# Performance work log

Hardware: AMD Instinct MI355X
Metric: run time of the kernel (lower is better)

## Reference

```python
import jax, jax.numpy as jnp
import numpy as np

N = 50000          # nodes
E = 1_600_000      # edges (avg degree 32)
F_IN = 128         # num_node_features
HID = 128          # hidden_dim
G = 512            # graphs in batch
NEG_SLOPE = 0.2    # PyG GATConv default


def setup_inputs() -> dict:
    key = jax.random.key(0)
    ks = jax.random.split(key, 13)
    s_in = 1.0 / np.sqrt(F_IN)
    s_h = 1.0 / np.sqrt(HID)
    return {
        "x": jax.random.normal(ks[0], (N, F_IN), jnp.float32),
        "edge_index": jax.random.randint(ks[1], (2, E), 0, N, dtype=jnp.int32),
        "batch": jnp.sort(jax.random.randint(ks[2], (N,), 0, G, dtype=jnp.int32)),
        "W1": jax.random.normal(ks[3], (F_IN, HID), jnp.float32) * s_in,
        "a_src1": jax.random.normal(ks[4], (HID,), jnp.float32) * s_h,
        "a_dst1": jax.random.normal(ks[5], (HID,), jnp.float32) * s_h,
        "b1": jnp.zeros((HID,), jnp.float32),
        "W2": jax.random.normal(ks[6], (HID, HID), jnp.float32) * s_h,
        "a_src2": jax.random.normal(ks[7], (HID,), jnp.float32) * s_h,
        "a_dst2": jax.random.normal(ks[8], (HID,), jnp.float32) * s_h,
        "b2": jnp.zeros((HID,), jnp.float32),
        "fc_w": jax.random.normal(ks[9], (2 * HID, 1), jnp.float32) * (1.0 / np.sqrt(2 * HID)),
        "fc_b": jnp.zeros((1,), jnp.float32),
    }


def _gat_conv(x, W, a_src, a_dst, b, src, dst, n):
    # PyG GATConv, heads=1: h = xW; alpha_e = softmax_dst(leaky_relu(a_s.h[src] + a_d.h[dst]))
    h = x @ W                                    # [N, C]
    asrc = h @ a_src                             # [N]
    adst = h @ a_dst                             # [N]
    logits = jax.nn.leaky_relu(asrc[src] + adst[dst], NEG_SLOPE)  # [E']
    m = jax.ops.segment_max(logits, dst, num_segments=n)
    ex = jnp.exp(logits - m[dst])
    denom = jax.ops.segment_sum(ex, dst, num_segments=n)
    alpha = ex / denom[dst]                      # segment softmax over incoming edges
    out = jax.ops.segment_sum(h[src] * alpha[:, None], dst, num_segments=n)
    return out + b


def reference(x, edge_index, batch, W1, a_src1, a_dst1, b1, W2, a_src2, a_dst2, b2, fc_w, fc_b):
    n = x.shape[0]
    loop = jnp.arange(n, dtype=edge_index.dtype)   # add_self_loops=True (PyG default)
    src = jnp.concatenate([edge_index[0], loop])
    dst = jnp.concatenate([edge_index[1], loop])

    h = jax.nn.relu(x)
    h = jax.nn.relu(_gat_conv(h, W1, a_src1, a_dst1, b1, src, dst, n))
    h = jax.nn.relu(_gat_conv(h, W2, a_src2, a_dst2, b2, src, dst, n))

    counts = jax.ops.segment_sum(jnp.ones((n,), h.dtype), batch, num_segments=G)
    maxp = jax.ops.segment_max(h, batch, num_segments=G)
    maxp = jnp.where(counts[:, None] > 0, maxp, 0.0)
    meanp = jax.ops.segment_sum(h, batch, num_segments=G) / jnp.maximum(counts, 1.0)[:, None]
    pooled = jnp.concatenate([maxp, meanp], axis=1)  # [G, 2*HID]
    return pooled @ fc_w + fc_b                      # [G, 1]
```

## Files before the change

### kernel.cpp

```cpp
#include <hip/hip_runtime.h>
#include <math.h>


#define LEAKY 0.2f
#define CAP 128
#define CSTRIDE 16

__device__ __forceinline__ unsigned short f2bf(float x) {
    unsigned int u = __float_as_uint(x);
    unsigned int r = (u + 0x7FFFu + ((u >> 16) & 1u)) >> 16;
    return (unsigned short)r;
}
__device__ __forceinline__ float bf2f(unsigned short b) {
    return __uint_as_float((unsigned int)b << 16);
}

__global__ __launch_bounds__(256) void gemmscat(const float* __restrict__ A,
                                                const float* __restrict__ B,
                                                float* __restrict__ C,
                                                unsigned short* __restrict__ Cb,
                                                const float* __restrict__ a_src,
                                                const float* __restrict__ a_dst,
                                                float* __restrict__ asv,
                                                float* __restrict__ adv,
                                                int n, int applyRelu,
                                                int gemmBlocks,
                                                const int* __restrict__ ei,
                                                int* __restrict__ cnt,
                                                unsigned short* __restrict__ col,
                                                int E) {
    __shared__ __align__(16) char smem[25600];
    float (*Ast)[68]  = (float(*)[68])smem;
    float (*Bs)[132]  = (float(*)[132])(smem + 8704);
    float (*sredS)[17] = (float(*)[17])smem;
    float (*sredD)[17] = (float(*)[17])(smem + 4352);

    if ((int)blockIdx.x >= gemmBlocks) {
        const int b = (int)blockIdx.x - gemmBlocks;
        const int g = (int)blockIdx.x & 7;
        const int lo = (int)(((long long)n * g) >> 3);
        const int hi = (int)(((long long)n * (g + 1)) >> 3);
        const int base = (b >> 3) * 4096;
        int4 dv[4], sv[4];
        int ok[4];
#pragma unroll
        for (int t = 0; t < 4; ++t) {
            int i0 = base + t * 1024 + (int)threadIdx.x * 4;
            ok[t] = (i0 < E);
            if (ok[t]) {
                dv[t] = *(const int4*)(ei + (size_t)E + i0);
                sv[t] = *(const int4*)(ei + i0);
            }
        }
#pragma unroll
        for (int t = 0; t < 4; ++t) {
            if (!ok[t]) continue;
            int dd[4] = { dv[t].x, dv[t].y, dv[t].z, dv[t].w };
            int ss[4] = { sv[t].x, sv[t].y, sv[t].z, sv[t].w };
#pragma unroll
            for (int j = 0; j < 4; ++j) {
                int d = dd[j];
                if (d >= lo && d < hi) {
                    int pos = atomicAdd(&cnt[(size_t)d * CSTRIDE], 1);
                    if (pos < CAP) col[(size_t)d * CAP + pos] = (unsigned short)ss[j];
                }
            }
        }
        return;
    }

    const int tid = threadIdx.x;
    const int row0 = blockIdx.x * 64;
    const int tx = tid & 15;
    const int ty = tid >> 4;
    float acc[4][8] = {};

    for (int k0 = 0; k0 < 128; k0 += 32) {
        {
            int kv = tid & 7, r = tid >> 3;
            int kk = kv * 4;
#pragma unroll
            for (int i = 0; i < 2; ++i) {
                int rr = r + 32 * i;
                int grow = row0 + rr;
                float4 v = make_float4(0.f, 0.f, 0.f, 0.f);
                if (grow < n) {
                    v = *(const float4*)(A + (size_t)grow * 128 + k0 + kk);
                    if (applyRelu) {
                        v.x = fmaxf(v.x, 0.f); v.y = fmaxf(v.y, 0.f);
                        v.z = fmaxf(v.z, 0.f); v.w = fmaxf(v.w, 0.f);
                    }
                }
                Ast[kk + 0][rr] = v.x;
                Ast[kk + 1][rr] = v.y;
                Ast[kk + 2][rr] = v.z;
                Ast[kk + 3][rr] = v.w;
            }
        }
        {
            int cv = tid & 31, kr = tid >> 5;
#pragma unroll
            for (int i = 0; i < 4; ++i) {
                int kk2 = kr + 8 * i;
                float4 v = *(const float4*)(B + (size_t)(k0 + kk2) * 128 + cv * 4);
                Bs[kk2][cv * 4 + 0] = v.x; Bs[kk2][cv * 4 + 1] = v.y;
                Bs[kk2][cv * 4 + 2] = v.z; Bs[kk2][cv * 4 + 3] = v.w;
            }
        }
        __syncthreads();
#pragma unroll
        for (int k = 0; k < 32; ++k) {
            float4 a4 = *(const float4*)&Ast[k][ty * 4];
            float4 q0 = *(const float4*)&Bs[k][tx * 8];
            float4 q1 = *(const float4*)&Bs[k][tx * 8 + 4];
            float a[4] = { a4.x, a4.y, a4.z, a4.w };
            float b[8] = { q0.x, q0.y, q0.z, q0.w, q1.x, q1.y, q1.z, q1.w };
#pragma unroll
            for (int i = 0; i < 4; ++i)
#pragma unroll
                for (int j = 0; j < 8; ++j) acc[i][j] += a[i] * b[j];
        }
        __syncthreads();
    }

    float asl[8], adl[8];
#pragma unroll
    for (int j = 0; j < 8; ++j) {
        asl[j] = a_src[tx * 8 + j];
        adl[j] = a_dst[tx * 8 + j];
    }
#pragma unroll
    for (int i = 0; i < 4; ++i) {
        int rr = ty * 4 + i;
        int grow = row0 + rr;
        float ps = 0.f, pd = 0.f;
#pragma unroll
        for (int j = 0; j < 8; ++j) {
            ps += acc[i][j] * asl[j];
            pd += acc[i][j] * adl[j];
        }
        sredS[rr][tx] = ps;
        sredD[rr][tx] = pd;
        if (grow < n) {
            float4* dst = (float4*)(C + (size_t)grow * 128 + tx * 8);
            dst[0] = make_float4(acc[i][0], acc[i][1], acc[i][2], acc[i][3]);
            dst[1] = make_float4(acc[i][4], acc[i][5], acc[i][6], acc[i][7]);
            uint4 pk;
            pk.x = (unsigned)f2bf(acc[i][0]) | ((unsigned)f2bf(acc[i][1]) << 16);
            pk.y = (unsigned)f2bf(acc[i][2]) | ((unsigned)f2bf(acc[i][3]) << 16);
            pk.z = (unsigned)f2bf(acc[i][4]) | ((unsigned)f2bf(acc[i][5]) << 16);
            pk.w = (unsigned)f2bf(acc[i][6]) | ((unsigned)f2bf(acc[i][7]) << 16);
            *(uint4*)(Cb + (size_t)grow * 128 + tx * 8) = pk;
        }
    }
    __syncthreads();
    if (tid < 64) {
        int grow = row0 + tid;
        if (grow < n) {
            float ps = 0.f, pd = 0.f;
#pragma unroll
            for (int j = 0; j < 16; ++j) {
                ps += sredS[tid][j];
                pd += sredD[tid][j];
            }
            asv[grow] = ps;
            adv[grow] = pd;
        }
    }
}

__global__ __launch_bounds__(256) void aggregate(const unsigned short* __restrict__ hb,
                                                 const int* __restrict__ cnt,
                                                 const unsigned short* __restrict__ col,
                                                 const float* __restrict__ asv,
                                                 const float* __restrict__ adv,
                                                 const float* __restrict__ bias,
                                                 float* __restrict__ out, int n) {
    __shared__ int   scol[4][128];
    __shared__ float swt[4][128];
    const int wv = threadIdx.x >> 6;
    const int lane = threadIdx.x & 63;
    const int w = blockIdx.x * 4 + wv;
    if (w >= n) return;
    int deg = cnt[(size_t)w * CSTRIDE];
    if (deg > CAP - 1) deg = CAP - 1;
    const int D = deg + 1;
    const size_t start = (size_t)w * CAP;
    const float ad = adv[w];

    int c0 = 0, c1 = 0;
    float l0 = -INFINITY, l1 = -INFINITY;
    if (lane < D) {
        c0 = (lane < deg) ? (int)col[start + lane] : w;
        l0 = asv[c0] + ad;
        l0 = l0 > 0.f ? l0 : LEAKY * l0;
    }
    if (64 + lane < D) {
        c1 = (64 + lane < deg) ? (int)col[start + 64 + lane] : w;
        l1 = asv[c1] + ad;
        l1 = l1 > 0.f ? l1 : LEAKY * l1;
    }
    float m = fmaxf(l0, l1);
#pragma unroll
    for (int off = 32; off; off >>= 1) m = fmaxf(m, __shfl_xor(m, off, 64));
    float e0 = (lane < D) ? __expf(l0 - m) : 0.f;
    float e1 = (64 + lane < D) ? __expf(l1 - m) : 0.f;
    float s = e0 + e1;
#pragma unroll
    for (int off = 32; off; off >>= 1) s += __shfl_xor(s, off, 64);
    float inv = 1.f / s;
    if (lane < D)      { scol[wv][lane] = c0;      swt[wv][lane] = e0; }
    if (64 + lane < D) { scol[wv][64 + lane] = c1; swt[wv][64 + lane] = e1; }

    const int hw = lane >> 5;
    const int sl = lane & 31;
    float4 aa[8];
#pragma unroll
    for (int j = 0; j < 8; ++j) aa[j] = make_float4(0.f, 0.f, 0.f, 0.f);
    for (int i = 0; i < D; i += 16) {
        int cs[8]; float ws[8];
#pragma unroll
        for (int j = 0; j < 8; ++j) {
            int idx = i + 2 * j + hw;
            int cl = idx < D ? idx : D - 1;
            cs[j] = scol[wv][cl];
            ws[j] = (idx < D) ? swt[wv][idx] : 0.f;
        }
        ushort4 rs[8];
#pragma unroll
        for (int j = 0; j < 8; ++j)
            rs[j] = *((const ushort4*)(hb + (size_t)cs[j] * 128) + sl);
#pragma unroll
        for (int j = 0; j < 8; ++j) {
            aa[j].x += ws[j] * bf2f(rs[j].x);
            aa[j].y += ws[j] * bf2f(rs[j].y);
            aa[j].z += ws[j] * bf2f(rs[j].z);
            aa[j].w += ws[j] * bf2f(rs[j].w);
        }
    }
#pragma unroll
    for (int j = 1; j < 8; ++j) {
        aa[0].x += aa[j].x; aa[0].y += aa[j].y;
        aa[0].z += aa[j].z; aa[0].w += aa[j].w;
    }
    aa[0].x += __shfl_xor(aa[0].x, 32);
    aa[0].y += __shfl_xor(aa[0].y, 32);
    aa[0].z += __shfl_xor(aa[0].z, 32);
    aa[0].w += __shfl_xor(aa[0].w, 32);
    if (hw == 0) {
        float4 b = ((const float4*)bias)[sl];
        float4 o;
        o.x = fmaxf(aa[0].x * inv + b.x, 0.f);
        o.y = fmaxf(aa[0].y * inv + b.y, 0.f);
        o.z = fmaxf(aa[0].z * inv + b.z, 0.f);
        o.w = fmaxf(aa[0].w * inv + b.w, 0.f);
        *((float4*)(out + (size_t)w * 128) + sl) = o;
    }
}

__global__ __launch_bounds__(128) void poolfc(const float* __restrict__ h2,
                                              const int* __restrict__ batch,
                                              const float* __restrict__ fcw,
                                              const float* __restrict__ fcb,
                                              float* __restrict__ out, int G, int n) {
    __shared__ int seg[2];
    int g = blockIdx.x;
    int f = threadIdx.x;
    if (f < 2) {
        int target = g + f;
        int lo = 0, hi = n;
        while (lo < hi) {
            int mid = (lo + hi) >> 1;
            if (batch[mid] < target) lo = mid + 1; else hi = mid;
        }
        seg[f] = lo;
    }
    __syncthreads();
    int s = seg[0], e = seg[1];
    float m = -INFINITY, sum = 0.f;
    for (int node = s; node < e; ++node) {
        float v = h2[(size_t)node * 128 + f];
        m = fmaxf(m, v);
        sum += v;
    }
    int cnt = e - s;
    float maxp = (cnt > 0) ? m : 0.f;
    float cden = (float)(cnt > 0 ? cnt : 1);
    float meanp = sum / cden;
    float p = maxp * fcw[f] + meanp * fcw[128 + f];
    __shared__ float red[128];
    red[f] = p;
    __syncthreads();
    for (int off = 64; off; off >>= 1) {
        if (f < off) red[f] += red[f + off];
        __syncthreads();
    }
    if (f == 0) out[g] = red[0] + fcb[0];
}

extern "C" void kernel_launch(void* const* d_in, const int* in_sizes, int n_in,
                              void* d_out, int out_size, void* d_ws, size_t ws_size,
                              hipStream_t stream) {
    const int N = in_sizes[0] / 128;
    const int E = in_sizes[1] / 2;
    const int G = out_size;

    const float* x      = (const float*)d_in[0];
    const int*   ei     = (const int*)d_in[1];
    const int*   batch  = (const int*)d_in[2];
    const float* W1     = (const float*)d_in[3];
    const float* a_src1 = (const float*)d_in[4];
    const float* a_dst1 = (const float*)d_in[5];
    const float* b1     = (const float*)d_in[6];
    const float* W2     = (const float*)d_in[7];
    const float* a_src2 = (const float*)d_in[8];
    const float* a_dst2 = (const float*)d_in[9];
    const float* b2     = (const float*)d_in[10];
    const float* fcw    = (const float*)d_in[11];
    const float* fcb    = (const float*)d_in[12];
    float* out = (float*)d_out;

    char* wp = (char*)d_ws;
    auto alloc = [&](size_t bytes) -> void* {
        void* p = (void*)wp;
        wp += (bytes + 255) & ~(size_t)255;
        return p;
    };
    int* cnt     = (int*)alloc(sizeof(int) * (size_t)N * CSTRIDE);
    unsigned short* col = (unsigned short*)alloc(sizeof(unsigned short) * (size_t)N * CAP);
    float* hp    = (float*)alloc(sizeof(float) * (size_t)N * 128);
    float* ha    = (float*)alloc(sizeof(float) * (size_t)N * 128);
    unsigned short* hb = (unsigned short*)alloc(sizeof(unsigned short) * (size_t)N * 128);
    float* asv   = (float*)alloc(sizeof(float) * N);
    float* adv   = (float*)alloc(sizeof(float) * N);

    hipMemsetAsync(cnt, 0, sizeof(int) * (size_t)N * CSTRIDE, stream);

    const int gemmGrid = (N + 63) / 64;
    const int waveGrid = (N + 3) / 4;
    const int scatGrid = ((E + 4095) / 4096) * 8;

    gemmscat<<<gemmGrid + scatGrid, 256, 0, stream>>>(
        x, W1, hp, hb, a_src1, a_dst1, asv, adv, N, 1, gemmGrid, ei, cnt, col, E);
    aggregate<<<waveGrid, 256, 0, stream>>>(hb, cnt, col, asv, adv, b1, ha, N);

    gemmscat<<<gemmGrid, 256, 0, stream>>>(
        ha, W2, hp, hb, a_src2, a_dst2, asv, adv, N, 0, gemmGrid, ei, cnt, col, E);
    aggregate<<<waveGrid, 256, 0, stream>>>(hb, cnt, col, asv, adv, b2, ha, N);

    poolfc<<<G, 128, 0, stream>>>(ha, batch, fcw, fcb, out, G, N);
}
```

Baseline: 359.3 us.

## Replace FP32 FMA GEMM with split-bf16 MFMA and drop fp32 h output

Result: faster. 352.0 us (-2.0%).

```diff
diff --git a/kernel.cpp b/kernel.cpp
--- a/kernel.cpp
+++ b/kernel.cpp
@@ -5,6 +5,9 @@
 #define LEAKY 0.2f
 #define CAP 128
 #define CSTRIDE 16
+
+typedef short bf16x8 __attribute__((ext_vector_type(8)));
+typedef float f32x4 __attribute__((ext_vector_type(4)));
 
 __device__ __forceinline__ unsigned short f2bf(float x) {
     unsigned int u = __float_as_uint(x);
@@ -15,25 +18,20 @@
     return __uint_as_float((unsigned int)b << 16);
 }
 
-__global__ __launch_bounds__(256) void gemmscat(const float* __restrict__ A,
-                                                const float* __restrict__ B,
-                                                float* __restrict__ C,
-                                                unsigned short* __restrict__ Cb,
-                                                const float* __restrict__ a_src,
-                                                const float* __restrict__ a_dst,
-                                                float* __restrict__ asv,
-                                                float* __restrict__ adv,
-                                                int n, int applyRelu,
-                                                int gemmBlocks,
-                                                const int* __restrict__ ei,
-                                                int* __restrict__ cnt,
-                                                unsigned short* __restrict__ col,
-                                                int E) {
-    __shared__ __align__(16) char smem[25600];
-    float (*Ast)[68]  = (float(*)[68])smem;
-    float (*Bs)[132]  = (float(*)[132])(smem + 8704);
-    float (*sredS)[17] = (float(*)[17])smem;
-    float (*sredD)[17] = (float(*)[17])(smem + 4352);
+__global__ __launch_bounds__(256, 5) void gemmscat(
+        const float* __restrict__ A,
+        const float* __restrict__ W,
+        unsigned short* __restrict__ Cb,
+        const float* __restrict__ a_src,
+        const float* __restrict__ a_dst,
+        float* __restrict__ asv,
+        float* __restrict__ adv,
+        int n, int applyRelu, int gemmBlocks,
+        const int* __restrict__ ei,
+        int* __restrict__ cnt,
+        unsigned short* __restrict__ col,
+        int E) {
+    __shared__ __align__(16) unsigned short Bt[2][64 * 128];
 
     if ((int)blockIdx.x >= gemmBlocks) {
         const int b = (int)blockIdx.x - gemmBlocks;
@@ -70,101 +68,132 @@
     }
 
     const int tid = threadIdx.x;
+    const int wv = tid >> 6;
+    const int lane = tid & 63;
+    const int cl = lane & 15;
+    const int kg = lane >> 4;
+
     const int row0 = blockIdx.x * 64;
-    const int tx = tid & 15;
-    const int ty = tid >> 4;
-    float acc[4][8] = {};
-
-    for (int k0 = 0; k0 < 128; k0 += 32) {
+    const int row = row0 + wv * 16 + cl;
+    bf16x8 ahi[4], alo[4];
+#pragma unroll
+    for (int ks = 0; ks < 4; ++ks) {
+        int k0 = ks * 32 + kg * 8;
+        float vv[8] = {0.f, 0.f, 0.f, 0.f, 0.f, 0.f, 0.f, 0.f};
+        if (row < n) {
+            float4 v0 = *(const float4*)(A + (size_t)row * 128 + k0);
+            float4 v1 = *(const float4*)(A + (size_t)row * 128 + k0 + 4);
+            vv[0] = v0.x; vv[1] = v0.y; vv[2] = v0.z; vv[3] = v0.w;
+            vv[4] = v1.x; vv[5] = v1.y; vv[6] = v1.z; vv[7] = v1.w;
+            if (applyRelu) {
+#pragma unroll
+                for (int u = 0; u < 8; ++u) vv[u] = fmaxf(vv[u], 0.f);
+            }
+        }
+#pragma unroll
+        for (int u = 0; u < 8; ++u) {
+            unsigned short h = f2bf(vv[u]);
+            ahi[ks][u] = (short)h;
+            alo[ks][u] = (short)f2bf(vv[u] - bf2f(h));
+        }
+    }
+
+    f32x4 acc[8];
+#pragma unroll
+    for (int ci = 0; ci < 8; ++ci) {
+        acc[ci][0] = 0.f; acc[ci][1] = 0.f; acc[ci][2] = 0.f; acc[ci][3] = 0.f;
+    }
+
+#pragma unroll
+    for (int h = 0; h < 2; ++h) {
+        __syncthreads();
         {
-            int kv = tid & 7, r = tid >> 3;
-            int kk = kv * 4;
-#pragma unroll
-            for (int i = 0; i < 2; ++i) {
-                int rr = r + 32 * i;
-                int grow = row0 + rr;
-                float4 v = make_float4(0.f, 0.f, 0.f, 0.f);
-                if (grow < n) {
-                    v = *(const float4*)(A + (size_t)grow * 128 + k0 + kk);
-                    if (applyRelu) {
-                        v.x = fmaxf(v.x, 0.f); v.y = fmaxf(v.y, 0.f);
-                        v.z = fmaxf(v.z, 0.f); v.w = fmaxf(v.w, 0.f);
-                    }
+            int c64 = tid & 63;
+            int c = h * 64 + c64;
+            int kh = tid >> 6;
+#pragma unroll
+            for (int j = 0; j < 4; ++j) {
+                int kb = kh * 32 + j * 8;
+                unsigned short thi[8], tlo[8];
+#pragma unroll
+                for (int u = 0; u < 8; ++u) {
+                    float v = W[(size_t)(kb + u) * 128 + c];
+                    unsigned short hh = f2bf(v);
+                    thi[u] = hh;
+                    tlo[u] = f2bf(v - bf2f(hh));
                 }
-                Ast[kk + 0][rr] = v.x;
-                Ast[kk + 1][rr] = v.y;
-                Ast[kk + 2][rr] = v.z;
-                Ast[kk + 3][rr] = v.w;
-            }
-        }
-        {
-            int cv = tid & 31, kr = tid >> 5;
-#pragma unroll
-            for (int i = 0; i < 4; ++i) {
-                int kk2 = kr + 8 * i;
-                float4 v = *(const float4*)(B + (size_t)(k0 + kk2) * 128 + cv * 4);
-                Bs[kk2][cv * 4 + 0] = v.x; Bs[kk2][cv * 4 + 1] = v.y;
-                Bs[kk2][cv * 4 + 2] = v.z; Bs[kk2][cv * 4 + 3] = v.w;
+                int byteoff = (c64 * 256 + kb * 2) ^ ((c64 & 7) << 4);
+                *(uint4*)((char*)Bt[0] + byteoff) = *(const uint4*)thi;
+                *(uint4*)((char*)Bt[1] + byteoff) = *(const uint4*)tlo;
             }
         }
         __syncthreads();
 #pragma unroll
-        for (int k = 0; k < 32; ++k) {
-            float4 a4 = *(const float4*)&Ast[k][ty * 4];
-            float4 q0 = *(const float4*)&Bs[k][tx * 8];
-            float4 q1 = *(const float4*)&Bs[k][tx * 8 + 4];
-            float a[4] = { a4.x, a4.y, a4.z, a4.w };
-            float b[8] = { q0.x, q0.y, q0.z, q0.w, q1.x, q1.y, q1.z, q1.w };
-#pragma unroll
-            for (int i = 0; i < 4; ++i)
-#pragma unroll
-                for (int j = 0; j < 8; ++j) acc[i][j] += a[i] * b[j];
-        }
-        __syncthreads();
-    }
-
-    float asl[8], adl[8];
-#pragma unroll
-    for (int j = 0; j < 8; ++j) {
-        asl[j] = a_src[tx * 8 + j];
-        adl[j] = a_dst[tx * 8 + j];
-    }
-#pragma unroll
-    for (int i = 0; i < 4; ++i) {
-        int rr = ty * 4 + i;
-        int grow = row0 + rr;
-        float ps = 0.f, pd = 0.f;
-#pragma unroll
-        for (int j = 0; j < 8; ++j) {
-            ps += acc[i][j] * asl[j];
-            pd += acc[i][j] * adl[j];
-        }
-        sredS[rr][tx] = ps;
-        sredD[rr][tx] = pd;
+        for (int ks = 0; ks < 4; ++ks) {
+            int k0 = ks * 32 + kg * 8;
+#pragma unroll
+            for (int ct = 0; ct < 4; ++ct) {
+                int c64 = ct * 16 + cl;
+                int byteoff = (c64 * 256 + k0 * 2) ^ ((c64 & 7) << 4);
+                bf16x8 bhi = *(const bf16x8*)((const char*)Bt[0] + byteoff);
+                bf16x8 blo = *(const bf16x8*)((const char*)Bt[1] + byteoff);
+                int ci = h * 4 + ct;
+                acc[ci] = __builtin_amdgcn_mfma_f32_16x16x32_bf16(
+                    ahi[ks], bhi, acc[ci], 0, 0, 0);
+                acc[ci] = __builtin_amdgcn_mfma_f32_16x16x32_bf16(
+                    ahi[ks], blo, acc[ci], 0, 0, 0);
+                acc[ci] = __builtin_amdgcn_mfma_f32_16x16x32_bf16(
+                    alo[ks], bhi, acc[ci], 0, 0, 0);
+            }
+        }
+    }
+
+    {
+        float ps[4] = {0.f, 0.f, 0.f, 0.f};
+        float pd[4] = {0.f, 0.f, 0.f, 0.f};
+#pragma unroll
+        for (int ci = 0; ci < 8; ++ci) {
+            float as_ = a_src[ci * 16 + cl];
+            float ad_ = a_dst[ci * 16 + cl];
+#pragma unroll
+            for (int r = 0; r < 4; ++r) {
+                ps[r] += acc[ci][r] * as_;
+                pd[r] += acc[ci][r] * ad_;
+            }
+        }
+#pragma unroll
+        for (int r = 0; r < 4; ++r) {
+#pragma unroll
+            for (int off = 1; off < 16; off <<= 1) {
+                ps[r] += __shfl_xor(ps[r], off, 64);
+                pd[r] += __shfl_xor(pd[r], off, 64);
+            }
+        }
+        if (cl == 0) {
+#pragma unroll
+            for (int r = 0; r < 4; ++r) {
+                int rr = row0 + wv * 16 + kg * 4 + r;
+                if (rr < n) { asv[rr] = ps[r]; adv[rr] = pd[r]; }
+            }
+        }
+    }
+
+    __syncthreads();
+    unsigned short* Cst = Bt[0];
+#pragma unroll
+    for (int ci = 0; ci < 8; ++ci) {
+#pragma unroll
+        for (int r = 0; r < 4; ++r)
+            Cst[(wv * 16 + kg * 4 + r) * 128 + ci * 16 + cl] = f2bf(acc[ci][r]);
+    }
+    __syncthreads();
+    {
+        int r = tid >> 2, cb = (tid & 3) * 32;
+        int grow = row0 + r;
         if (grow < n) {
-            float4* dst = (float4*)(C + (size_t)grow * 128 + tx * 8);
-            dst[0] = make_float4(acc[i][0], acc[i][1], acc[i][2], acc[i][3]);
-            dst[1] = make_float4(acc[i][4], acc[i][5], acc[i][6], acc[i][7]);
-            uint4 pk;
-            pk.x = (unsigned)f2bf(acc[i][0]) | ((unsigned)f2bf(acc[i][1]) << 16);
-            pk.y = (unsigned)f2bf(acc[i][2]) | ((unsigned)f2bf(acc[i][3]) << 16);
-            pk.z = (unsigned)f2bf(acc[i][4]) | ((unsigned)f2bf(acc[i][5]) << 16);
-            pk.w = (unsigned)f2bf(acc[i][6]) | ((unsigned)f2bf(acc[i][7]) << 16);
-            *(uint4*)(Cb + (size_t)grow * 128 + tx * 8) = pk;
-        }
-    }
-    __syncthreads();
-    if (tid < 64) {
-        int grow = row0 + tid;
-        if (grow < n) {
-            float ps = 0.f, pd = 0.f;
-#pragma unroll
-            for (int j = 0; j < 16; ++j) {
-                ps += sredS[tid][j];
-                pd += sredD[tid][j];
-            }
-            asv[grow] = ps;
-            adv[grow] = pd;
+            uint4* dst = (uint4*)(Cb + (size_t)grow * 128 + cb);
+            const uint4* src = (const uint4*)(Cst + r * 128 + cb);
+            dst[0] = src[0]; dst[1] = src[1]; dst[2] = src[2]; dst[3] = src[3];
         }
     }
 }
@@ -328,7 +357,6 @@
     };
     int* cnt     = (int*)alloc(sizeof(int) * (size_t)N * CSTRIDE);
     unsigned short* col = (unsigned short*)alloc(sizeof(unsigned short) * (size_t)N * CAP);
-    float* hp    = (float*)alloc(sizeof(float) * (size_t)N * 128);
     float* ha    = (float*)alloc(sizeof(float) * (size_t)N * 128);
     unsigned short* hb = (unsigned short*)alloc(sizeof(unsigned short) * (size_t)N * 128);
     float* asv   = (float*)alloc(sizeof(float) * N);
@@ -341,11 +369,11 @@
     const int scatGrid = ((E + 4095) / 4096) * 8;
 
     gemmscat<<<gemmGrid + scatGrid, 256, 0, stream>>>(
-        x, W1, hp, hb, a_src1, a_dst1, asv, adv, N, 1, gemmGrid, ei, cnt, col, E);
+        x, W1, hb, a_src1, a_dst1, asv, adv, N, 1, gemmGrid, ei, cnt, col, E);
     aggregate<<<waveGrid, 256, 0, stream>>>(hb, cnt, col, asv, adv, b1, ha, N);
 
     gemmscat<<<gemmGrid, 256, 0, stream>>>(
-        ha, W2, hp, hb, a_src2, a_dst2, asv, adv, N, 0, gemmGrid, ei, cnt, col, E);
+        ha, W2, hb, a_src2, a_dst2, asv, adv, N, 0, gemmGrid, ei, cnt, col, E);
     aggregate<<<waveGrid, 256, 0, stream>>>(hb, cnt, col, asv, adv, b2, ha, N);
 
     poolfc<<<G, 128, 0, stream>>>(ha, batch, fcw, fcb, out, G, N);
```
